# Performance work log

Measured on AMD Instinct MI355X. Metric: run time of the kernel, lower is better.

Reference implementation:

```python
import jax, jax.numpy as jnp
import numpy as np

B, N, NE = 2, 100000, 800000
S, F, D = 3, 2, 128          # space_size, n_fields, enc_dim
TD, CD, SD = 11, 32, 10      # enc_t_dim, cond_dim, spatial_dim


def _mlp(x, w1, b1, w2, b2):
    # Linear -> SiLU -> Linear (MLP with n_hidden=1, hidden=128, no layernorm)
    return jax.nn.silu(x @ w1 + b1) @ w2 + b2


def setup_inputs() -> dict:
    key = jax.random.key(0)
    ks = iter(jax.random.split(key, 40))

    def w(shape):
        fan_in = shape[-2] if len(shape) >= 2 else shape[-1]
        return jax.random.normal(next(ks), shape, jnp.float32) / np.sqrt(fan_in)

    def b(shape):
        return jnp.zeros(shape, jnp.float32)

    inp = dict(
        node_pos=jax.random.normal(next(ks), (B, N, S), jnp.float32),
        state_in=jax.random.normal(next(ks), (B, N, F), jnp.float32),
        time_i=jax.random.normal(next(ks), (B, TD), jnp.float32),
        conditions=jax.random.normal(next(ks), (B, CD), jnp.float32),
        spatial_inform=jax.random.normal(next(ks), (B, SD), jnp.float32),
        edges=jax.random.randint(next(ks), (B, NE, 2), 0, N, jnp.int64)
        if jax.config.jax_enable_x64 else jax.random.randint(next(ks), (B, NE, 2), 0, N, jnp.int32),
        # per-field node MLPs, stacked over fields: input = space_size + 1
        fields_w1=w((F, S + 1, D)), fields_b1=b((F, D)),
        fields_w2=w((F, D, D)), fields_b2=b((F, D)),
        # time / cond / spatial MLPs
        time_w1=w((TD, D)), time_b1=b((D,)), time_w2=w((D, D)), time_b2=b((D,)),
        cond_w1=w((CD, D)), cond_b1=b((D,)), cond_w2=w((D, D)), cond_b2=b((D,)),
        spat_w1=w((SD, D)), spat_b1=b((D,)), spat_w2=w((D, D)), spat_b2=b((D,)),
        # fuse_para: 3*D -> 128 -> 2*D
        fuse_w1=w((3 * D, D)), fuse_b1=b((D,)),
        fuse_w2=w((D, 2 * D)), fuse_b2=b((2 * D,)),
        # edge MLP: 2*S+1 -> 128 -> D
        fe_w1=w((2 * S + 1, D)), fe_b1=b((D,)),
        fe_w2=w((D, D)), fe_b2=b((D,)),
    )
    return inp


def reference(node_pos, state_in, time_i, conditions, spatial_inform, edges,
              fields_w1, fields_b1, fields_w2, fields_b2,
              time_w1, time_b1, time_w2, time_b2,
              cond_w1, cond_b1, cond_w2, cond_b2,
              spat_w1, spat_b1, spat_w2, spat_b2,
              fuse_w1, fuse_b1, fuse_w2, fuse_b2,
              fe_w1, fe_b1, fe_w2, fe_b2):
    # FiLM parameters from time + condition + spatial encodings
    time_enc = _mlp(time_i, time_w1, time_b1, time_w2, time_b2)        # [B,D]
    cond_enc = _mlp(conditions, cond_w1, cond_b1, cond_w2, cond_b2)    # [B,D]
    spat_enc = _mlp(spatial_inform, spat_w1, spat_b1, spat_w2, spat_b2)
    h = jnp.concatenate([cond_enc, time_enc, spat_enc], axis=-1)       # [B,3D]
    para = _mlp(h, fuse_w1, fuse_b1, fuse_w2, fuse_b2)                 # [B,2D]
    gamma, beta = jnp.split(para, 2, axis=-1)                          # [B,D] each

    # Per-field node MLPs, vectorized over fields: x_f [B,N,F,S+1]
    pos_b = jnp.broadcast_to(node_pos[:, :, None, :], (node_pos.shape[0], node_pos.shape[1], F, S))
    x_f = jnp.concatenate([pos_b, state_in[..., None]], axis=-1)       # [B,N,F,S+1]
    hid = jax.nn.silu(jnp.einsum('bnfd,fde->bnfe', x_f, fields_w1) + fields_b1)
    V = jnp.einsum('bnfe,feo->bnfo', hid, fields_w2) + fields_b2       # [B,N,F,D]
    V = V * gamma[:, None, None, :] + beta[:, None, None, :]

    # Edge features: gather sender/receiver positions, diff/norm/concat
    idx_s = jnp.broadcast_to(edges[..., 0:1], edges.shape[:2] + (S,))
    idx_r = jnp.broadcast_to(edges[..., 1:2], edges.shape[:2] + (S,))
    senders = jnp.take_along_axis(node_pos, idx_s, axis=1)             # [B,NE,S]
    receivers = jnp.take_along_axis(node_pos, idx_r, axis=1)
    d = receivers - senders
    norm = jnp.sqrt(jnp.sum(d * d, axis=-1, keepdims=True) + 1e-8)
    e_feat = jnp.concatenate([d, -d, norm], axis=-1)                   # [B,NE,2S+1]
    E = _mlp(e_feat, fe_w1, fe_b1, fe_w2, fe_b2)                       # [B,NE,D]

    return V, E
```

## Files before the change

kernel.cpp:

```cpp
#include <hip/hip_runtime.h>
#include <hip/hip_bf16.h>
#include <string.h>

#define B_  2
#define N_  100000
#define NE_ 800000
#define F_  2
#define D_  128
#define TD_ 11
#define CD_ 32
#define SD_ 10

#define NODE_BX   782
#define NODE_NB   (NODE_BX * F_ * B_)
#define EDGE_BX   6250
#define EDGE_NB   (EDGE_BX * B_)
#define GROUPS    3125
#define TOTAL_NB  (NODE_NB + EDGE_NB)

#define WS_GB      0
#define WS_FLAG    2048
#define WS_W1FRAG  2112
#define WS_W2FRAG  26688

typedef short s16x8 __attribute__((ext_vector_type(8)));
typedef float f32x4 __attribute__((ext_vector_type(4)));
typedef unsigned u32x4 __attribute__((ext_vector_type(4)));

static __device__ __forceinline__ unsigned short f2bf(float f) {
    unsigned u = __builtin_bit_cast(unsigned, f);
    u += 0x7FFFu + ((u >> 16) & 1u);
    return (unsigned short)(u >> 16);
}
static __device__ __forceinline__ float silu_f(float x) {
    return x * __builtin_amdgcn_rcpf(1.0f + __expf(-x));
}
static __device__ __forceinline__ unsigned pack_bf16(float lo, float hi) {
    __hip_bfloat162 c = __float22bfloat162_rn(make_float2(lo, hi));
    unsigned r;
    memcpy(&r, &c, sizeof(r));
    return r;
}
static __device__ __forceinline__ void lds_barrier() {
    asm volatile("s_waitcnt lgkmcnt(0)" ::: "memory");
    __builtin_amdgcn_s_barrier();
}

__global__ void prep_kernel(
    const float* __restrict__ time_i, const float* __restrict__ cond,
    const float* __restrict__ spat,
    const float* tw1, const float* tb1, const float* tw2, const float* tb2,
    const float* cw1, const float* cb1, const float* cw2, const float* cb2,
    const float* sw1, const float* sb1, const float* sw2, const float* sb2,
    const float* fuw1, const float* fub1, const float* fuw2, const float* fub2,
    const float* __restrict__ fw1, const float* __restrict__ fb1,
    const float* __restrict__ fw2,
    const float* __restrict__ ew1, const float* __restrict__ eb1,
    const float* __restrict__ ew2,
    const int* __restrict__ edges,
    char* __restrict__ ws)
{
    const int bx = blockIdx.x, t = threadIdx.x;

    if (bx < 2) {
        const int b = bx, d = t;
        __shared__ float h[3 * D_];
        __shared__ float hid[D_];

        const float* X [3] = { cond + b * CD_, time_i + b * TD_, spat + b * SD_ };
        const float* W1[3] = { cw1, tw1, sw1 };
        const float* B1[3] = { cb1, tb1, sb1 };
        const float* W2[3] = { cw2, tw2, sw2 };
        const float* B2[3] = { cb2, tb2, sb2 };
        const int    K [3] = { CD_, TD_, SD_ };

        for (int m = 0; m < 3; ++m) {
            float a = 0.f;
            if (d < D_) {
                a = B1[m][d];
                for (int k = 0; k < K[m]; ++k) a += X[m][k] * W1[m][k * D_ + d];
            }
            __syncthreads();
            if (d < D_) hid[d] = a / (1.0f + __expf(-a));
            __syncthreads();
            if (d < D_) {
                float o = B2[m][d];
                for (int k = 0; k < D_; ++k) o += hid[k] * W2[m][k * D_ + d];
                h[m * D_ + d] = o;
            }
        }
        __syncthreads();
        float pre2 = 0.f;
        if (d < D_) {
            pre2 = fub1[d];
            for (int k = 0; k < 3 * D_; ++k) pre2 += h[k] * fuw1[k * D_ + d];
        }
        __syncthreads();
        if (d < D_) hid[d] = pre2 / (1.0f + __expf(-pre2));
        __syncthreads();
        if (d < D_) {
            float g = fub2[d], be = fub2[D_ + d];
            for (int k = 0; k < D_; ++k) {
                float hv = hid[k];
                g  += hv * fuw2[k * 2 * D_ + d];
                be += hv * fuw2[k * 2 * D_ + D_ + d];
            }
            float* gb = (float*)ws;
            gb[(b * 2 + 0) * D_ + d] = g;
            gb[(b * 2 + 1) * D_ + d] = be;
        }
    } else if (bx < 5) {
        const int which = bx - 2;
        const float* src = (which < 2) ? (fw2 + which * D_ * D_) : ew2;
        unsigned short* dst = (unsigned short*)(ws + WS_W2FRAG) + (long)which * 2048 * 8;
        for (int e = t; e < 2048; e += 256) {
            const int lanee = e & 63, kb = (e >> 6) & 3, nt = e >> 8;
            const int out = nt * 16 + (lanee & 15);
            const int kgA = lanee >> 4;
            s16x8 v;
            #pragma unroll
            for (int i = 0; i < 8; ++i) {
                const int hid = kb * 32 + ((i >> 2) << 4) + kgA * 4
                              + (((i >> 1) & 1) << 1) + (i & 1);
                v[i] = (short)f2bf(src[hid * D_ + out]);
            }
            *(s16x8*)(dst + e * 8) = v;
        }
    } else {
        if (t == 0) {
            int nz = 0;
            for (int j = 0; j < 64; ++j) nz |= edges[2 * j + 1];
            ((float*)(ws + WS_FLAG))[0] = (nz == 0) ? 1.0f : 0.0f;
        }
        unsigned short* w1f = (unsigned short*)(ws + WS_W1FRAG);
        for (int e = t; e < 1536; e += 256) {
            const int which = e >> 9;
            const int h8    = (e >> 6) & 7;
            const int lane  = e & 63;
            const int m  = h8 * 16 + (lane & 15);
            const int kg = lane >> 4;
            s16x8 v;
            #pragma unroll
            for (int i = 0; i < 8; ++i) {
                const int k = kg * 8 + i;
                float val = 0.f;
                if (kg == 0) {
                    if (which < 2) {
                        if (k < 4)      val = fw1[(which * 4 + k) * D_ + m];
                        else if (k == 4) val = fb1[which * D_ + m];
                    } else {
                        if (k < 3)      val = ew1[k * D_ + m] - ew1[(k + 3) * D_ + m];
                        else if (k == 3) val = ew1[6 * D_ + m];
                        else if (k == 4) val = eb1[m];
                    }
                }
                v[i] = (short)f2bf(val);
            }
            *(s16x8*)(w1f + e * 8) = v;
        }
    }
}

__global__ __launch_bounds__(256, 3) void fused_kernel(
    const float* __restrict__ pos, const float* __restrict__ state,
    const int* __restrict__ edges,
    const float* __restrict__ fb2, const float* __restrict__ eb2,
    const char* __restrict__ ws,
    float* __restrict__ V, float* __restrict__ E)
{
    __shared__ __align__(16) char smem[34816];
    unsigned short* w2lds = (unsigned short*)smem;
    float* outF = (float*)smem;

    const int bx = blockIdx.x, t = threadIdx.x;
    const int lane = t & 63, wv = t >> 6;
    const int kg = lane >> 4, lr = lane & 15;

    const float* gbAll = (const float*)ws;
    const char*  w1fB  = ws + WS_W1FRAG;
    const unsigned short* w2all = (const unsigned short*)(ws + WS_W2FRAG);

    bool isNode; int sub;
    if (bx >= 5 * GROUPS) { isNode = true; sub = GROUPS + (bx - 5 * GROUPS); }
    else {
        int g = bx / 5, s = bx - 5 * g;
        if (s == 0) { isNode = true;  sub = g; }
        else        { isNode = false; sub = g * 4 + (s - 1); }
    }

    float xa[4], xb[4];
    int n0 = 0, f = 0, b, e0blk = 0;
    if (isNode) {
        n0 = (sub % NODE_BX) * 128;
        f  = (sub / NODE_BX) & 1;
        b  = sub / (NODE_BX * F_);
        int na = n0 + wv * 32 + lr;      if (na >= N_) na = N_ - 1;
        int nb = n0 + wv * 32 + lr + 16; if (nb >= N_) nb = N_ - 1;
        long pa = ((long)b * N_ + na) * 3, pb = ((long)b * N_ + nb) * 3;
        xa[0] = pos[pa]; xa[1] = pos[pa + 1]; xa[2] = pos[pa + 2];
        xb[0] = pos[pb]; xb[1] = pos[pb + 1]; xb[2] = pos[pb + 2];
        xa[3] = state[((long)b * N_ + na) * F_ + f];
        xb[3] = state[((long)b * N_ + nb) * F_ + f];
    } else {
        e0blk = (sub % EDGE_BX) * 128;
        b     = sub / EDGE_BX;
        const bool x64 = ((const float*)(ws + WS_FLAG))[0] > 0.5f;
        const long ea = (long)b * NE_ + e0blk + wv * 32 + lr;
        const long eb = ea + 16;
        int sa, ra, sb, rb;
        if (x64) {
            sa = edges[ea * 4]; ra = edges[ea * 4 + 2];
            sb = edges[eb * 4]; rb = edges[eb * 4 + 2];
        } else {
            int2 va = *(const int2*)(edges + ea * 2); sa = va.x; ra = va.y;
            int2 vb = *(const int2*)(edges + eb * 2); sb = vb.x; rb = vb.y;
        }
        const float* pp = pos + (long)b * N_ * 3;
        {
            long so = (long)sa * 3, ro = (long)ra * 3;
            xa[0] = pp[ro]     - pp[so];
            xa[1] = pp[ro + 1] - pp[so + 1];
            xa[2] = pp[ro + 2] - pp[so + 2];
            xa[3] = sqrtf(xa[0]*xa[0] + xa[1]*xa[1] + xa[2]*xa[2] + 1e-8f);
        }
        {
            long so = (long)sb * 3, ro = (long)rb * 3;
            xb[0] = pp[ro]     - pp[so];
            xb[1] = pp[ro + 1] - pp[so + 1];
            xb[2] = pp[ro + 2] - pp[so + 2];
            xb[3] = sqrtf(xb[0]*xb[0] + xb[1]*xb[1] + xb[2]*xb[2] + 1e-8f);
        }
    }

    const int which = isNode ? f : 2;

    {
        const char* src = (const char*)(w2all + (long)which * 2048 * 8);
        #pragma unroll
        for (int j = 0; j < 8; ++j) {
            f32x4 v = *(const f32x4*)(src + (j * 256 + t) * 16);
            *(f32x4*)((char*)w2lds + (j * 256 + t) * 16) = v;
        }
    }
    __syncthreads();

    const char* w1fr = w1fB + which * 8192;
    const f32x4 zero4 = (f32x4){0.f, 0.f, 0.f, 0.f};

    uint2 d0[8], d1[8];
    {
        s16x8 bop0, bop1;
        {
            u32x4 bf;
            bf[0] = pack_bf16(xa[0], xa[1]); bf[1] = pack_bf16(xa[2], xa[3]);
            bf[2] = 0x00003F80u;             bf[3] = 0u;
            memcpy(&bop0, &bf, sizeof(bop0));
            bf[0] = pack_bf16(xb[0], xb[1]); bf[1] = pack_bf16(xb[2], xb[3]);
            memcpy(&bop1, &bf, sizeof(bop1));
        }
        #pragma unroll
        for (int h8 = 0; h8 < 8; ++h8) {
            s16x8 af = *(const s16x8*)(w1fr + h8 * 1024 + lane * 16);
            f32x4 h4 = __builtin_amdgcn_mfma_f32_16x16x32_bf16(af, bop0, zero4, 0, 0, 0);
            f32x4 g4 = __builtin_amdgcn_mfma_f32_16x16x32_bf16(af, bop1, zero4, 0, 0, 0);
            d0[h8].x = pack_bf16(silu_f(h4[0]), silu_f(h4[1]));
            d0[h8].y = pack_bf16(silu_f(h4[2]), silu_f(h4[3]));
            d1[h8].x = pack_bf16(silu_f(g4[0]), silu_f(g4[1]));
            d1[h8].y = pack_bf16(silu_f(g4[2]), silu_f(g4[3]));
        }
    }

    f32x4 acc[2][8];
    #pragma unroll
    for (int rt = 0; rt < 2; ++rt)
        #pragma unroll
        for (int nt = 0; nt < 8; ++nt) acc[rt][nt] = (f32x4){0.f, 0.f, 0.f, 0.f};

    #pragma unroll
    for (int kb = 0; kb < 4; ++kb) {
        s16x8 u0, u1;
        {
            u32x4 uw;
            uw[0] = d0[2 * kb].x;     uw[1] = d0[2 * kb].y;
            uw[2] = d0[2 * kb + 1].x; uw[3] = d0[2 * kb + 1].y;
            memcpy(&u0, &uw, sizeof(u0));
            uw[0] = d1[2 * kb].x;     uw[1] = d1[2 * kb].y;
            uw[2] = d1[2 * kb + 1].x; uw[3] = d1[2 * kb + 1].y;
            memcpy(&u1, &uw, sizeof(u1));
        }
        #pragma unroll
        for (int nt = 0; nt < 8; ++nt) {
            s16x8 afr = *(const s16x8*)(w2lds + ((nt * 4 + kb) * 64 + lane) * 8);
            acc[0][nt] = __builtin_amdgcn_mfma_f32_16x16x32_bf16(afr, u0, acc[0][nt], 0, 0, 0);
            acc[1][nt] = __builtin_amdgcn_mfma_f32_16x16x32_bf16(afr, u1, acc[1][nt], 0, 0, 0);
        }
    }

    const float* bias  = isNode ? (fb2 + f * D_) : eb2;
    const float* gamma = gbAll + b * 2 * D_;
    const float* beta  = gamma + D_;
    float* base = isNode ? (V + (((long)b * N_ + n0) * F_ + f) * D_)
                         : (E + ((long)b * NE_ + e0blk) * D_);
    const long stride   = isNode ? (long)F_ * D_ : (long)D_;
    const int rowsValid = isNode ? (N_ - n0) : 128;

    lds_barrier();

    #pragma unroll
    for (int p = 0; p < 2; ++p) {
        #pragma unroll
        for (int ntl = 0; ntl < 4; ++ntl) {
            const int nt = p * 4 + ntl;
            const int d0c = nt * 16 + kg * 4;
            const f32x4 bs = *(const f32x4*)(bias + d0c);
            f32x4 g, be;
            if (isNode) { g = *(const f32x4*)(gamma + d0c); be = *(const f32x4*)(beta + d0c); }
            #pragma unroll
            for (int mt = 0; mt < 2; ++mt) {
                const int m = wv * 32 + mt * 16 + lr;
                f32x4 v;
                #pragma unroll
                for (int r = 0; r < 4; ++r)
                    v[r] = isNode ? (acc[mt][nt][r] + bs[r]) * g[r] + be[r]
                                  : acc[mt][nt][r] + bs[r];
                *(f32x4*)(outF + m * 68 + ntl * 16 + kg * 4) = v;
            }
        }
        lds_barrier();
        #pragma unroll
        for (int j = 0; j < 8; ++j) {
            const int r = wv * 32 + j * 4 + (lane >> 4);
            const int c = (lane & 15) * 4;
            f32x4 v = *(const f32x4*)(outF + r * 68 + c);
            if (r < rowsValid)
                __builtin_nontemporal_store(v, (f32x4*)(base + (long)r * stride + p * 64 + c));
        }
        if (p == 0) lds_barrier();
    }
}

extern "C" void kernel_launch(void* const* d_in, const int* in_sizes, int n_in,
                              void* d_out, int out_size, void* d_ws, size_t ws_size,
                              hipStream_t stream)
{
    (void)in_sizes; (void)n_in; (void)out_size; (void)ws_size;

    const float* node_pos  = (const float*)d_in[0];
    const float* state_in  = (const float*)d_in[1];
    const float* time_i    = (const float*)d_in[2];
    const float* conditions= (const float*)d_in[3];
    const float* spatial   = (const float*)d_in[4];
    const int*   edges     = (const int*)d_in[5];
    const float* fields_w1 = (const float*)d_in[6];
    const float* fields_b1 = (const float*)d_in[7];
    const float* fields_w2 = (const float*)d_in[8];
    const float* fields_b2 = (const float*)d_in[9];
    const float* tw1 = (const float*)d_in[10];
    const float* tb1 = (const float*)d_in[11];
    const float* tw2 = (const float*)d_in[12];
    const float* tb2 = (const float*)d_in[13];
    const float* cw1 = (const float*)d_in[14];
    const float* cb1 = (const float*)d_in[15];
    const float* cw2 = (const float*)d_in[16];
    const float* cb2 = (const float*)d_in[17];
    const float* sw1 = (const float*)d_in[18];
    const float* sb1 = (const float*)d_in[19];
    const float* sw2 = (const float*)d_in[20];
    const float* sb2 = (const float*)d_in[21];
    const float* fu_w1 = (const float*)d_in[22];
    const float* fu_b1 = (const float*)d_in[23];
    const float* fu_w2 = (const float*)d_in[24];
    const float* fu_b2 = (const float*)d_in[25];
    const float* fe_w1 = (const float*)d_in[26];
    const float* fe_b1 = (const float*)d_in[27];
    const float* fe_w2 = (const float*)d_in[28];
    const float* fe_b2 = (const float*)d_in[29];

    char*  ws = (char*)d_ws;
    float* V  = (float*)d_out;
    float* E  = V + (long)B_ * N_ * F_ * D_;

    prep_kernel<<<dim3(6), dim3(256), 0, stream>>>(
        time_i, conditions, spatial,
        tw1, tb1, tw2, tb2, cw1, cb1, cw2, cb2, sw1, sb1, sw2, sb2,
        fu_w1, fu_b1, fu_w2, fu_b2,
        fields_w1, fields_b1, fields_w2,
        fe_w1, fe_b1, fe_w2,
        edges, ws);

    fused_kernel<<<dim3(TOTAL_NB), dim3(256), 0, stream>>>(
        node_pos, state_in, edges, fields_b2, fe_b2, ws, V, E);
}
```

Measured before the change: 231.2 us.

## Read W2 fragments from global memory, drop LDS staging and block barriers

W2 MFMA operand fragments are now read directly from the global workspace (L1/L2-cached) instead of being staged into LDS behind a block-wide __syncthreads. The second GEMM is split into two halves matching the output passes, which halves the live accumulators, and occupancy is raised to 4 blocks. Each wave only touches its own rows of the LDS output tile, so the block barriers become per-wave waitcnt fences. The risk is more global/L2 traffic and added latency on the MFMA operand loads.

```diff
diff --git a/kernel.cpp b/kernel.cpp
--- a/kernel.cpp
+++ b/kernel.cpp
@@ -41,9 +41,8 @@
     memcpy(&r, &c, sizeof(r));
     return r;
 }
-static __device__ __forceinline__ void lds_barrier() {
+static __device__ __forceinline__ void wave_fence() {
     asm volatile("s_waitcnt lgkmcnt(0)" ::: "memory");
-    __builtin_amdgcn_s_barrier();
 }
 
 __global__ void prep_kernel(
@@ -161,16 +160,14 @@
     }
 }
 
-__global__ __launch_bounds__(256, 3) void fused_kernel(
+__global__ __launch_bounds__(256, 4) void fused_kernel(
     const float* __restrict__ pos, const float* __restrict__ state,
     const int* __restrict__ edges,
     const float* __restrict__ fb2, const float* __restrict__ eb2,
     const char* __restrict__ ws,
     float* __restrict__ V, float* __restrict__ E)
 {
-    __shared__ __align__(16) char smem[34816];
-    unsigned short* w2lds = (unsigned short*)smem;
-    float* outF = (float*)smem;
+    __shared__ __align__(16) float outF[128 * 68];
 
     const int bx = blockIdx.x, t = threadIdx.x;
     const int lane = t & 63, wv = t >> 6;
@@ -178,7 +175,6 @@
 
     const float* gbAll = (const float*)ws;
     const char*  w1fB  = ws + WS_W1FRAG;
-    const unsigned short* w2all = (const unsigned short*)(ws + WS_W2FRAG);
 
     bool isNode; int sub;
     if (bx >= 5 * GROUPS) { isNode = true; sub = GROUPS + (bx - 5 * GROUPS); }
@@ -233,18 +229,9 @@
     }
 
     const int which = isNode ? f : 2;
-
-    {
-        const char* src = (const char*)(w2all + (long)which * 2048 * 8);
-        #pragma unroll
-        for (int j = 0; j < 8; ++j) {
-            f32x4 v = *(const f32x4*)(src + (j * 256 + t) * 16);
-            *(f32x4*)((char*)w2lds + (j * 256 + t) * 16) = v;
-        }
-    }
-    __syncthreads();
-
     const char* w1fr = w1fB + which * 8192;
+    const s16x8* w2p = ((const s16x8*)(ws + WS_W2FRAG))
+                     + (long)which * 2048 + lane;
     const f32x4 zero4 = (f32x4){0.f, 0.f, 0.f, 0.f};
 
     uint2 d0[8], d1[8];
@@ -270,32 +257,6 @@
         }
     }
 
-    f32x4 acc[2][8];
-    #pragma unroll
-    for (int rt = 0; rt < 2; ++rt)
-        #pragma unroll
-        for (int nt = 0; nt < 8; ++nt) acc[rt][nt] = (f32x4){0.f, 0.f, 0.f, 0.f};
-
-    #pragma unroll
-    for (int kb = 0; kb < 4; ++kb) {
-        s16x8 u0, u1;
-        {
-            u32x4 uw;
-            uw[0] = d0[2 * kb].x;     uw[1] = d0[2 * kb].y;
-            uw[2] = d0[2 * kb + 1].x; uw[3] = d0[2 * kb + 1].y;
-            memcpy(&u0, &uw, sizeof(u0));
-            uw[0] = d1[2 * kb].x;     uw[1] = d1[2 * kb].y;
-            uw[2] = d1[2 * kb + 1].x; uw[3] = d1[2 * kb + 1].y;
-            memcpy(&u1, &uw, sizeof(u1));
-        }
-        #pragma unroll
-        for (int nt = 0; nt < 8; ++nt) {
-            s16x8 afr = *(const s16x8*)(w2lds + ((nt * 4 + kb) * 64 + lane) * 8);
-            acc[0][nt] = __builtin_amdgcn_mfma_f32_16x16x32_bf16(afr, u0, acc[0][nt], 0, 0, 0);
-            acc[1][nt] = __builtin_amdgcn_mfma_f32_16x16x32_bf16(afr, u1, acc[1][nt], 0, 0, 0);
-        }
-    }
-
     const float* bias  = isNode ? (fb2 + f * D_) : eb2;
     const float* gamma = gbAll + b * 2 * D_;
     const float* beta  = gamma + D_;
@@ -304,29 +265,54 @@
     const long stride   = isNode ? (long)F_ * D_ : (long)D_;
     const int rowsValid = isNode ? (N_ - n0) : 128;
 
-    lds_barrier();
-
     #pragma unroll
     for (int p = 0; p < 2; ++p) {
+        f32x4 acc[2][4];
+        #pragma unroll
+        for (int rt = 0; rt < 2; ++rt)
+            #pragma unroll
+            for (int ntl = 0; ntl < 4; ++ntl) acc[rt][ntl] = zero4;
+
+        #pragma unroll
+        for (int kb = 0; kb < 4; ++kb) {
+            s16x8 u0, u1;
+            {
+                u32x4 uw;
+                uw[0] = d0[2 * kb].x;     uw[1] = d0[2 * kb].y;
+                uw[2] = d0[2 * kb + 1].x; uw[3] = d0[2 * kb + 1].y;
+                memcpy(&u0, &uw, sizeof(u0));
+                uw[0] = d1[2 * kb].x;     uw[1] = d1[2 * kb].y;
+                uw[2] = d1[2 * kb + 1].x; uw[3] = d1[2 * kb + 1].y;
+                memcpy(&u1, &uw, sizeof(u1));
+            }
+            #pragma unroll
+            for (int ntl = 0; ntl < 4; ++ntl) {
+                const int nt = p * 4 + ntl;
+                s16x8 afr = w2p[(nt * 4 + kb) * 64];
+                acc[0][ntl] = __builtin_amdgcn_mfma_f32_16x16x32_bf16(afr, u0, acc[0][ntl], 0, 0, 0);
+                acc[1][ntl] = __builtin_amdgcn_mfma_f32_16x16x32_bf16(afr, u1, acc[1][ntl], 0, 0, 0);
+            }
+        }
+
         #pragma unroll
         for (int ntl = 0; ntl < 4; ++ntl) {
-            const int nt = p * 4 + ntl;
-            const int d0c = nt * 16 + kg * 4;
-            const f32x4 bs = *(const f32x4*)(bias + d0c);
+            const int gc = (p * 4 + ntl) * 16 + kg * 4;
+            const int lc = ntl * 16 + kg * 4;
+            const f32x4 bs = *(const f32x4*)(bias + gc);
             f32x4 g, be;
-            if (isNode) { g = *(const f32x4*)(gamma + d0c); be = *(const f32x4*)(beta + d0c); }
+            if (isNode) { g = *(const f32x4*)(gamma + gc); be = *(const f32x4*)(beta + gc); }
             #pragma unroll
             for (int mt = 0; mt < 2; ++mt) {
                 const int m = wv * 32 + mt * 16 + lr;
                 f32x4 v;
                 #pragma unroll
                 for (int r = 0; r < 4; ++r)
-                    v[r] = isNode ? (acc[mt][nt][r] + bs[r]) * g[r] + be[r]
-                                  : acc[mt][nt][r] + bs[r];
-                *(f32x4*)(outF + m * 68 + ntl * 16 + kg * 4) = v;
-            }
-        }
-        lds_barrier();
+                    v[r] = isNode ? (acc[mt][ntl][r] + bs[r]) * g[r] + be[r]
+                                  : acc[mt][ntl][r] + bs[r];
+                *(f32x4*)(outF + m * 68 + lc) = v;
+            }
+        }
+        wave_fence();
         #pragma unroll
         for (int j = 0; j < 8; ++j) {
             const int r = wv * 32 + j * 4 + (lane >> 4);
@@ -335,7 +321,7 @@
             if (r < rowsValid)
                 __builtin_nontemporal_store(v, (f32x4*)(base + (long)r * stride + p * 64 + c));
         }
-        if (p == 0) lds_barrier();
+        wave_fence();
     }
 }
 
```

After: 370.3 us. 1.6x slower.
